# Kernel optimization log

Measured on AMD Instinct MI355X. Metric: run time of the kernel, lower is better.

The kernel has to match this reference:

```python
import jax, jax.numpy as jnp
import numpy as np

B, P, CIN, PS = 8192, 9, 12, 64   # batch, patches, channels, patch_size
D_IN = CIN * PS                    # 768 flattened patch features
ENC_H, D = 512, 1024               # patch_encoder_hidden, embedding_dim
E, EXP_H, C = 8, 2048, 1000        # num_experts, expert hidden, num_classes
SYM, SYM_H = 6, 64                 # symbolic_dim, symbolic gating hidden


def setup_inputs() -> dict:
    key = jax.random.key(0)
    ks = jax.random.split(key, 16)
    g = lambda k, shape, fan: jax.random.normal(k, shape, jnp.float32) / np.sqrt(fan)
    return {
        "patches": jax.random.normal(ks[0], (B, P, CIN, PS), jnp.float32),
        "symbolic_features": jax.random.normal(ks[1], (B, SYM), jnp.float32),
        # patch encoder (2-layer MLP per patch)
        "enc_w1": g(ks[2], (D_IN, ENC_H), D_IN), "enc_b1": jnp.zeros((ENC_H,), jnp.float32),
        "enc_w2": g(ks[3], (ENC_H, D), ENC_H),   "enc_b2": jnp.zeros((D,), jnp.float32),
        # neural gating: Linear(D,D)-ReLU-Linear(D,E)
        "gn_w1": g(ks[4], (D, D), D), "gn_b1": jnp.zeros((D,), jnp.float32),
        "gn_w2": g(ks[5], (D, E), D), "gn_b2": jnp.zeros((E,), jnp.float32),
        # symbolic gating: Linear(SYM,64)-ReLU-Linear(64,E)
        "gs_w1": g(ks[6], (SYM, SYM_H), SYM),  "gs_b1": jnp.zeros((SYM_H,), jnp.float32),
        "gs_w2": g(ks[7], (SYM_H, E), SYM_H),  "gs_b2": jnp.zeros((E,), jnp.float32),
        # stacked experts: Linear(D,H)-ReLU-(Dropout=eval identity)-Linear(H,C)
        "ew1": g(ks[8], (E, D, EXP_H), D),      "eb1": jnp.zeros((E, EXP_H), jnp.float32),
        "ew2": g(ks[9], (E, EXP_H, C), EXP_H),  "eb2": jnp.zeros((E, C), jnp.float32),
    }


def reference(patches, symbolic_features, enc_w1, enc_b1, enc_w2, enc_b2,
              gn_w1, gn_b1, gn_w2, gn_b2, gs_w1, gs_b1, gs_w2, gs_b2,
              ew1, eb1, ew2, eb2):
    b = patches.shape[0]
    # patch encoder: (b, P, CIN*PS) -> (b, P, D)
    x = patches.reshape(b, P, D_IN)
    h = jax.nn.relu(jnp.einsum('bpf,fh->bph', x, enc_w1) + enc_b1)
    encoded = jnp.einsum('bph,hd->bpd', h, enc_w2) + enc_b2
    # mean aggregation over patches
    agg = encoded.mean(axis=1)  # (b, D)
    # symbolic gating: 0.5*neural + 0.5*symbolic logits, softmax
    neural = jax.nn.relu(agg @ gn_w1 + gn_b1) @ gn_w2 + gn_b2            # (b, E)
    symb = jax.nn.relu(symbolic_features @ gs_w1 + gs_b1) @ gs_w2 + gs_b2  # (b, E)
    gating_weights = jax.nn.softmax(0.5 * neural + 0.5 * symb, axis=1)
    # all experts densely (batched over expert axis)
    eh = jax.nn.relu(jnp.einsum('bd,edh->beh', agg, ew1) + eb1)          # (b, E, H)
    expert_logits = jnp.einsum('beh,ehc->bec', eh, ew2) + eb2            # (b, E, C)
    # gate-weighted sum
    logits = jnp.einsum('be,bec->bc', gating_weights, expert_logits)     # (b, C)
    return logits, gating_weights, expert_logits
```

## Files before the change

### kernel.cpp

```cpp
#include <hip/hip_runtime.h>
#include <hip/hip_bf16.h>

typedef __attribute__((ext_vector_type(8))) short s16x8;
typedef __attribute__((ext_vector_type(4))) float f32x4;

#define DEV __device__ __forceinline__

DEV short f2b(float f) {
  __hip_bfloat16 h = __float2bfloat16(f);
  short s; __builtin_memcpy(&s, &h, 2); return s;
}
DEV float b2f(short s) {
  __hip_bfloat16 h; __builtin_memcpy(&h, &s, 2); return __bfloat162float(h);
}

typedef __attribute__((address_space(1))) const void gvoid;
typedef __attribute__((address_space(3))) void lvoid;
DEV void gload_lds16(const void* g, void* l) {
  __builtin_amdgcn_global_load_lds((gvoid*)g, (lvoid*)l, 16, 0, 0);
}

static constexpr int kB = 8192, kP = 9, kDIN = 768, kENCH = 512, kD = 1024;
static constexpr int kE = 8, kH = 2048, kC = 1000;
static constexpr size_t OUT_GATE   = (size_t)kB * kC;
static constexpr size_t OUT_EL     = OUT_GATE + (size_t)kB * kE;

static constexpr size_t W1T  = 0;
static constexpr size_t W2T  = W1T  + 786432;
static constexpr size_t GW1T = W2T  + 1048576;
static constexpr size_t EW1T = GW1T + 2097152;
static constexpr size_t EW2T = EW1T + 33554432;
static constexpr size_t PBF  = EW2T + 32768000;
static constexpr size_t HBUF = PBF  + 113246208;
static constexpr size_t EH4  = HBUF + 75497472;
static constexpr size_t HMEAN = PBF;
static constexpr size_t AGG   = HMEAN + 8388608;
static constexpr size_t GH    = AGG   + 16777216;
static constexpr size_t NEU   = GH    + 16777216;
static constexpr size_t SYMB  = NEU   + 262144;

__global__ void cast_bf16_kernel(const float* __restrict__ in, short* __restrict__ out, size_t n8) {
  size_t i = (size_t)blockIdx.x * blockDim.x + threadIdx.x;
  if (i >= n8) return;
  float4 a = ((const float4*)in)[i * 2];
  float4 b = ((const float4*)in)[i * 2 + 1];
  s16x8 v;
  v[0] = f2b(a.x); v[1] = f2b(a.y); v[2] = f2b(a.z); v[3] = f2b(a.w);
  v[4] = f2b(b.x); v[5] = f2b(b.y); v[6] = f2b(b.z); v[7] = f2b(b.w);
  *(s16x8*)(out + i * 8) = v;
}

__global__ void transpose_cast_kernel(const float* __restrict__ in, short* __restrict__ out,
                                      int R, int C, size_t istride, size_t ostride) {
  __shared__ float tile[32][33];
  const float* W = in + istride * blockIdx.z;
  short* T = out + ostride * blockIdx.z;
  int tx = threadIdx.x, ty = threadIdx.y;
  int c0 = blockIdx.x * 32, r0 = blockIdx.y * 32;
  #pragma unroll
  for (int i = 0; i < 32; i += 8) {
    int r = r0 + ty + i, c = c0 + tx;
    if (r < R && c < C) tile[ty + i][tx] = W[(size_t)r * C + c];
  }
  __syncthreads();
  #pragma unroll
  for (int i = 0; i < 32; i += 8) {
    int rr = c0 + ty + i, cc = r0 + tx;
    if (rr < C && cc < R) T[(size_t)rr * R + cc] = f2b(tile[tx][ty + i]);
  }
}

#define BARR() __builtin_amdgcn_s_barrier()
#define LGKM0() do { asm volatile("s_waitcnt lgkmcnt(0)" ::: "memory"); \
                     __builtin_amdgcn_sched_barrier(0); } while (0)
#define VMW4() asm volatile("s_waitcnt vmcnt(4)" ::: "memory")
#define VMW0() asm volatile("s_waitcnt vmcnt(0)" ::: "memory")

template<bool RELU, bool F32OUT, bool NTAIL>
__global__ __launch_bounds__(512, 2)
void gemm256_kernel(const short* __restrict__ A, const short* __restrict__ Bt,
                    const float* __restrict__ bias, void* __restrict__ Cout,
                    int M, int N, int K, int ldc,
                    long aZ, long bZ, long biasZ, long cZ) {
  __shared__ short Abuf[2][2][8192];
  __shared__ short Bbuf[2][2][8192];
  const int z = blockIdx.z;
  A += (size_t)z * aZ; Bt += (size_t)z * bZ; bias += (size_t)z * biasZ;

  const int XT = gridDim.x;
  int lid = blockIdx.y * XT + blockIdx.x;
  const int cpx = (XT * gridDim.y) >> 3;
  lid = (lid & 7) * cpx + (lid >> 3);
  const int bx = lid % XT, by = lid / XT;
  const int bM = by * 256, bN = bx * 256;

  const int t = threadIdx.x, lane = t & 63, wid = t >> 6;
  const int wm = wid & 1, wn = wid >> 1;
  const int lr = lane & 15, kg = lane >> 4;
  const int nkt = K >> 6;

  const int srB = t >> 3;
  const int sx = (t & 7) ^ (srB & 7);
  const int ldsoff = wid * 512;

#define STAGE_A(half, g_) do { \
    _Pragma("unroll") \
    for (int i_ = 0; i_ < 2; ++i_) { \
      int r_ = i_ * 64 + srB; \
      gload_lds16(A + (size_t)(bM + (half) * 128 + r_) * K + (g_) * 64 + sx * 8, \
                  &Abuf[(g_) & 1][half][i_ * 4096 + ldsoff]); \
    } } while (0)

#define STAGE_B(half, g_) do { \
    _Pragma("unroll") \
    for (int i_ = 0; i_ < 2; ++i_) { \
      int r_ = i_ * 64 + srB; \
      int row_ = bN + (half) * 128 + r_; \
      if (NTAIL && row_ >= N) row_ = N - 1; \
      gload_lds16(Bt + (size_t)row_ * K + (g_) * 64 + sx * 8, \
                  &Bbuf[(g_) & 1][half][i_ * 4096 + ldsoff]); \
    } } while (0)

  int aro = (wm * 64 + lr) * 64;
  int bro = (wn * 32 + lr) * 64;
  int so0 = ((0 * 4 + kg) ^ (lr & 7)) * 8;
  int so1 = ((1 * 4 + kg) ^ (lr & 7)) * 8;

  s16x8 af[4][2], bf[2][2];
#define LDA(mh, par_) do { \
    _Pragma("unroll") \
    for (int m_ = 0; m_ < 4; ++m_) { \
      af[m_][0] = *(const s16x8*)&Abuf[par_][mh][aro + m_ * 1024 + so0]; \
      af[m_][1] = *(const s16x8*)&Abuf[par_][mh][aro + m_ * 1024 + so1]; \
    } } while (0)
#define LDB(nh, par_) do { \
    _Pragma("unroll") \
    for (int n_ = 0; n_ < 2; ++n_) { \
      bf[n_][0] = *(const s16x8*)&Bbuf[par_][nh][bro + n_ * 1024 + so0]; \
      bf[n_][1] = *(const s16x8*)&Bbuf[par_][nh][bro + n_ * 1024 + so1]; \
    } } while (0)

  f32x4 acc[2][2][4][2];
  #pragma unroll
  for (int a_ = 0; a_ < 2; ++a_)
    #pragma unroll
    for (int b_ = 0; b_ < 2; ++b_)
      #pragma unroll
      for (int m_ = 0; m_ < 4; ++m_)
        #pragma unroll
        for (int n_ = 0; n_ < 2; ++n_) acc[a_][b_][m_][n_] = (f32x4){0.f, 0.f, 0.f, 0.f};

#define MMA(mh, nh) do { \
    __builtin_amdgcn_s_setprio(1); \
    _Pragma("unroll") \
    for (int m_ = 0; m_ < 4; ++m_) \
      _Pragma("unroll") \
      for (int n_ = 0; n_ < 2; ++n_) { \
        acc[mh][nh][m_][n_] = __builtin_amdgcn_mfma_f32_16x16x32_bf16(af[m_][0], bf[n_][0], acc[mh][nh][m_][n_], 0, 0, 0); \
        acc[mh][nh][m_][n_] = __builtin_amdgcn_mfma_f32_16x16x32_bf16(af[m_][1], bf[n_][1], acc[mh][nh][m_][n_], 0, 0, 0); \
      } \
    __builtin_amdgcn_s_setprio(0); } while (0)

  STAGE_A(0, 0); STAGE_B(0, 0); STAGE_B(1, 0); STAGE_A(1, 0);
  if (nkt > 1) { STAGE_A(0, 1); STAGE_B(1, 1); VMW4(); } else { VMW0(); }
  BARR();

  for (int g = 0; g < nkt; ++g) {
    const int par = g & 1;
    LDA(0, par); LDB(0, par);
    if (g + 1 < nkt) STAGE_B(0, g + 1);
    BARR(); LGKM0();
    MMA(0, 0);
    BARR();
    LDB(1, par);
    if (g + 1 < nkt) STAGE_A(1, g + 1);
    BARR(); LGKM0();
    MMA(0, 1);
    BARR();
    LDA(1, par);
    if (g + 2 < nkt) STAGE_A(0, g + 2);
    BARR(); LGKM0();
    MMA(1, 1);
    BARR();
    LDB(0, par);
    if (g + 2 < nkt) STAGE_B(1, g + 2);
    if (g < nkt - 2) { VMW4(); } else if (g == nkt - 2) { VMW0(); }
    BARR(); LGKM0();
    MMA(1, 0);
    BARR();
  }

  #pragma unroll
  for (int nh = 0; nh < 2; ++nh)
    #pragma unroll
    for (int n_ = 0; n_ < 2; ++n_) {
      int col = bN + nh * 128 + wn * 32 + n_ * 16 + lr;
      if (NTAIL && col >= N) continue;
      float bv = bias[col];
      #pragma unroll
      for (int mh = 0; mh < 2; ++mh)
        #pragma unroll
        for (int m_ = 0; m_ < 4; ++m_) {
          int row0 = bM + mh * 128 + wm * 64 + m_ * 16 + kg * 4;
          #pragma unroll
          for (int r_ = 0; r_ < 4; ++r_) {
            float v = acc[mh][nh][m_][n_][r_] + bv;
            if (RELU) v = fmaxf(v, 0.f);
            size_t off = (size_t)(row0 + r_) * ldc + col;
            if (F32OUT) ((float*)Cout + (size_t)z * cZ)[off] = v;
            else        ((short*)Cout + (size_t)z * cZ)[off] = f2b(v);
          }
        }
    }
#undef STAGE_A
#undef STAGE_B
#undef LDA
#undef LDB
#undef MMA
}

template<bool RELU, bool F32OUT>
__global__ __launch_bounds__(256, 2)
void gemm_bt_kernel(const short* __restrict__ A, const short* __restrict__ Bt,
                    const float* __restrict__ bias, void* __restrict__ Cout,
                    int M, int N, int K, int ldc) {
  __shared__ short As[128 * 32];
  __shared__ short Bs[128 * 32];
  const int t = threadIdx.x;
  const int lane = t & 63, wid = t >> 6;
  const int wr = wid >> 1, wc = wid & 1;
  const int lr = lane & 15, lk8 = (lane >> 4) * 8;
  const int arow0 = blockIdx.y * 128;
  const int bcol0 = blockIdx.x * 128;

  f32x4 acc[4][4];
  #pragma unroll
  for (int m = 0; m < 4; ++m)
    #pragma unroll
    for (int n = 0; n < 4; ++n) acc[m][n] = (f32x4){0.f, 0.f, 0.f, 0.f};

  const int srow = t >> 2, sseg = (t & 3) * 8;
  const short* ga0 = A + (size_t)(arow0 + srow) * K + sseg;
  const short* ga1 = ga0 + (size_t)64 * K;
  int br0 = bcol0 + srow;      if (br0 >= N) br0 = N - 1;
  int br1 = bcol0 + srow + 64; if (br1 >= N) br1 = N - 1;
  const short* gb0 = Bt + (size_t)br0 * K + sseg;
  const short* gb1 = Bt + (size_t)br1 * K + sseg;
  short* lA0 = As + wid * 512;
  short* lA1 = As + 2048 + wid * 512;
  short* lB0 = Bs + wid * 512;
  short* lB1 = Bs + 2048 + wid * 512;

  for (int k0 = 0; k0 < K; k0 += 32) {
    __syncthreads();
    gload_lds16(ga0, lA0);
    gload_lds16(ga1, lA1);
    gload_lds16(gb0, lB0);
    gload_lds16(gb1, lB1);
    ga0 += 32; ga1 += 32; gb0 += 32; gb1 += 32;
    __syncthreads();
    s16x8 af[4], bfr[4];
    #pragma unroll
    for (int m = 0; m < 4; ++m) af[m] = *(const s16x8*)&As[(wr * 64 + m * 16 + lr) * 32 + lk8];
    #pragma unroll
    for (int n = 0; n < 4; ++n) bfr[n] = *(const s16x8*)&Bs[(wc * 64 + n * 16 + lr) * 32 + lk8];
    #pragma unroll
    for (int m = 0; m < 4; ++m)
      #pragma unroll
      for (int n = 0; n < 4; ++n)
        acc[m][n] = __builtin_amdgcn_mfma_f32_16x16x32_bf16(af[m], bfr[n], acc[m][n], 0, 0, 0);
  }

  #pragma unroll
  for (int n = 0; n < 4; ++n) {
    int col = bcol0 + wc * 64 + n * 16 + lr;
    if (col >= N) continue;
    float bv = bias[col];
    #pragma unroll
    for (int m = 0; m < 4; ++m) {
      int row0 = arow0 + wr * 64 + m * 16 + (lane >> 4) * 4;
      #pragma unroll
      for (int r = 0; r < 4; ++r) {
        float v = acc[m][n][r] + bv;
        if (RELU) v = fmaxf(v, 0.f);
        size_t off = (size_t)(row0 + r) * ldc + col;
        if (F32OUT) ((float*)Cout)[off] = v;
        else        ((short*)Cout)[off] = f2b(v);
      }
    }
  }
}

__global__ void mean9_kernel(const short* __restrict__ h, short* __restrict__ hm) {
  size_t i = (size_t)blockIdx.x * blockDim.x + threadIdx.x;
  if (i >= (size_t)kB * kENCH / 8) return;
  size_t b = i >> 6; int d8 = (int)(i & 63);
  const short* base = h + b * kP * kENCH + d8 * 8;
  float s[8] = {0, 0, 0, 0, 0, 0, 0, 0};
  #pragma unroll
  for (int p = 0; p < kP; ++p) {
    s16x8 v = *(const s16x8*)(base + p * kENCH);
    #pragma unroll
    for (int j = 0; j < 8; ++j) s[j] += b2f(v[j]);
  }
  s16x8 o;
  #pragma unroll
  for (int j = 0; j < 8; ++j) o[j] = f2b(s[j] * (1.f / 9.f));
  *(s16x8*)(hm + i * 8) = o;
}

__global__ __launch_bounds__(256)
void gating_neural_kernel(const short* __restrict__ gh, const float* __restrict__ w2,
                          const float* __restrict__ b2, float* __restrict__ neural) {
  int wid = threadIdx.x >> 6, lane = threadIdx.x & 63;
  int row = blockIdx.x * 4 + wid;
  float acc[8] = {0,0,0,0,0,0,0,0};
  const short* grow = gh + (size_t)row * kD;
  for (int k = lane; k < kD; k += 64) {
    float x = b2f(grow[k]);
    const float* w = w2 + (size_t)k * 8;
    #pragma unroll
    for (int c = 0; c < 8; ++c) acc[c] += x * w[c];
  }
  #pragma unroll
  for (int c = 0; c < 8; ++c)
    #pragma unroll
    for (int off = 32; off >= 1; off >>= 1) acc[c] += __shfl_xor(acc[c], off);
  if (lane == 0) {
    #pragma unroll
    for (int c = 0; c < 8; ++c) neural[(size_t)row * 8 + c] = acc[c] + b2[c];
  }
}

__global__ __launch_bounds__(256)
void gating_symb_kernel(const float* __restrict__ sym, const float* __restrict__ w1,
                        const float* __restrict__ b1, const float* __restrict__ w2,
                        const float* __restrict__ b2, float* __restrict__ symb) {
  int wid = threadIdx.x >> 6, lane = threadIdx.x & 63;
  int row = blockIdx.x * 4 + wid;
  float s0 = sym[(size_t)row * 6 + 0], s1 = sym[(size_t)row * 6 + 1], s2 = sym[(size_t)row * 6 + 2];
  float s3 = sym[(size_t)row * 6 + 3], s4 = sym[(size_t)row * 6 + 4], s5 = sym[(size_t)row * 6 + 5];
  float hh = b1[lane];
  hh += s0 * w1[0 * 64 + lane] + s1 * w1[1 * 64 + lane] + s2 * w1[2 * 64 + lane];
  hh += s3 * w1[3 * 64 + lane] + s4 * w1[4 * 64 + lane] + s5 * w1[5 * 64 + lane];
  hh = fmaxf(hh, 0.f);
  float acc[8];
  #pragma unroll
  for (int c = 0; c < 8; ++c) acc[c] = hh * w2[lane * 8 + c];
  #pragma unroll
  for (int c = 0; c < 8; ++c)
    #pragma unroll
    for (int off = 32; off >= 1; off >>= 1) acc[c] += __shfl_xor(acc[c], off);
  if (lane == 0) {
    #pragma unroll
    for (int c = 0; c < 8; ++c) symb[(size_t)row * 8 + c] = acc[c] + b2[c];
  }
}

__global__ void gating_softmax_kernel(const float* __restrict__ neural, const float* __restrict__ symb,
                                      float* __restrict__ gate_out) {
  int row = blockIdx.x * blockDim.x + threadIdx.x;
  if (row >= kB) return;
  float g[8], m = -1e30f;
  #pragma unroll
  for (int c = 0; c < 8; ++c) {
    g[c] = 0.5f * (neural[(size_t)row * 8 + c] + symb[(size_t)row * 8 + c]);
    m = fmaxf(m, g[c]);
  }
  float sum = 0.f;
  #pragma unroll
  for (int c = 0; c < 8; ++c) { g[c] = expf(g[c] - m); sum += g[c]; }
  float inv = 1.f / sum;
  #pragma unroll
  for (int c = 0; c < 8; ++c) gate_out[(size_t)row * 8 + c] = g[c] * inv;
}

__global__ __launch_bounds__(256)
void combine_kernel(float* __restrict__ out) {
  int b = blockIdx.y;
  int c = blockIdx.x * 256 + threadIdx.x;
  __shared__ float g[8];
  if (threadIdx.x < 8) g[threadIdx.x] = out[OUT_GATE + (size_t)b * 8 + threadIdx.x];
  __syncthreads();
  if (c < kC) {
    const float* el = out + OUT_EL + (size_t)b * (kE * kC) + c;
    float a = 0.f;
    #pragma unroll
    for (int e = 0; e < 8; ++e) a += g[e] * el[e * kC];
    out[(size_t)b * kC + c] = a;
  }
}

static void launch_gemm128(bool relu, bool f32out, const short* A, const short* Bt, const float* bias,
                           void* C, int M, int N, int K, int ldc, hipStream_t s) {
  dim3 g((N + 127) / 128, M / 128), b(256);
  if (relu && !f32out)       gemm_bt_kernel<true,  false><<<g, b, 0, s>>>(A, Bt, bias, C, M, N, K, ldc);
  else if (!relu && !f32out) gemm_bt_kernel<false, false><<<g, b, 0, s>>>(A, Bt, bias, C, M, N, K, ldc);
  else if (relu && f32out)   gemm_bt_kernel<true,  true ><<<g, b, 0, s>>>(A, Bt, bias, C, M, N, K, ldc);
  else                       gemm_bt_kernel<false, true ><<<g, b, 0, s>>>(A, Bt, bias, C, M, N, K, ldc);
}

extern "C" void kernel_launch(void* const* d_in, const int* in_sizes, int n_in,
                              void* d_out, int out_size, void* d_ws, size_t ws_size,
                              hipStream_t stream) {
  const float* patches = (const float*)d_in[0];
  const float* symf    = (const float*)d_in[1];
  const float* enc_w1  = (const float*)d_in[2];
  const float* enc_b1  = (const float*)d_in[3];
  const float* enc_w2  = (const float*)d_in[4];
  const float* enc_b2  = (const float*)d_in[5];
  const float* gn_w1   = (const float*)d_in[6];
  const float* gn_b1   = (const float*)d_in[7];
  const float* gn_w2   = (const float*)d_in[8];
  const float* gn_b2   = (const float*)d_in[9];
  const float* gs_w1   = (const float*)d_in[10];
  const float* gs_b1   = (const float*)d_in[11];
  const float* gs_w2   = (const float*)d_in[12];
  const float* gs_b2   = (const float*)d_in[13];
  const float* ew1     = (const float*)d_in[14];
  const float* eb1     = (const float*)d_in[15];
  const float* ew2     = (const float*)d_in[16];
  const float* eb2     = (const float*)d_in[17];
  char* ws = (char*)d_ws;
  float* out = (float*)d_out;
  dim3 tb(32, 8);

  {
    size_t n8 = (size_t)kB * kP * kDIN / 8;
    cast_bf16_kernel<<<(unsigned)((n8 + 255) / 256), 256, 0, stream>>>(patches, (short*)(ws + PBF), n8);
  }
  transpose_cast_kernel<<<dim3(16, 24, 1), tb, 0, stream>>>(enc_w1, (short*)(ws + W1T),  kDIN,  kENCH, 0, 0);
  transpose_cast_kernel<<<dim3(32, 16, 1), tb, 0, stream>>>(enc_w2, (short*)(ws + W2T),  kENCH, kD,    0, 0);
  transpose_cast_kernel<<<dim3(32, 32, 1), tb, 0, stream>>>(gn_w1,  (short*)(ws + GW1T), kD,    kD,    0, 0);
  transpose_cast_kernel<<<dim3(64, 32, 8), tb, 0, stream>>>(ew1,    (short*)(ws + EW1T), kD,    kH,
                                                            (size_t)kD * kH, (size_t)kD * kH);
  transpose_cast_kernel<<<dim3(32, 64, 8), tb, 0, stream>>>(ew2,    (short*)(ws + EW2T), kH,    kC,
                                                            (size_t)kH * kC, (size_t)kH * kC);
  gemm256_kernel<true, false, false><<<dim3(2, 288, 1), 512, 0, stream>>>(
      (short*)(ws + PBF), (short*)(ws + W1T), enc_b1, ws + HBUF,
      kB * kP, kENCH, kDIN, kENCH, 0, 0, 0, 0);
  mean9_kernel<<<(kB * kENCH / 8) / 256, 256, 0, stream>>>((short*)(ws + HBUF), (short*)(ws + HMEAN));
  launch_gemm128(false, false, (short*)(ws + HMEAN), (short*)(ws + W2T), enc_b2,
                 ws + AGG, kB, kD, kENCH, kD, stream);
  launch_gemm128(true, false, (short*)(ws + AGG), (short*)(ws + GW1T), gn_b1,
                 ws + GH, kB, kD, kD, kD, stream);
  gating_neural_kernel<<<kB / 4, 256, 0, stream>>>((short*)(ws + GH), gn_w2, gn_b2, (float*)(ws + NEU));
  gating_symb_kernel<<<kB / 4, 256, 0, stream>>>(symf, gs_w1, gs_b1, gs_w2, gs_b2, (float*)(ws + SYMB));
  gating_softmax_kernel<<<kB / 256, 256, 0, stream>>>((float*)(ws + NEU), (float*)(ws + SYMB), out + OUT_GATE);
  for (int h = 0; h < 2; ++h) {
    int e0 = h * 4;
    gemm256_kernel<true, false, false><<<dim3(8, 32, 4), 512, 0, stream>>>(
        (short*)(ws + AGG), (short*)(ws + EW1T) + (size_t)e0 * kH * kD, eb1 + (size_t)e0 * kH,
        ws + EH4, kB, kH, kD, kH,
        0, (long)kH * kD, kH, (long)kB * kH);
    gemm256_kernel<false, true, true><<<dim3(4, 32, 4), 512, 0, stream>>>(
        (short*)(ws + EH4), (short*)(ws + EW2T) + (size_t)e0 * kC * kH, eb2 + (size_t)e0 * kC,
        out + OUT_EL + (size_t)e0 * kC, kB, kC, kH, kE * kC,
        (long)kB * kH, (long)kC * kH, kC, kC);
  }
  combine_kernel<<<dim3(4, kB), 256, 0, stream>>>(out);
}
```

Before: 1.033 ms.

## Keep B fragments in registers and issue unconditional prefetches with clamped indices

Gives the B fragment registers a per-half dimension so the final MMA(1,0) reuses the B(0) fragments loaded earlier, which drops one set of LDS reads per k-tile. Prefetch stages now always issue, with out-of-range tile indices clamped to the last tile. This keeps the number of outstanding loads constant so fixed vmcnt waits (8 and 6) can replace the conditional waits, placed at different points in the loop. It costs extra registers for the B fragments and some redundant global loads in the last iterations, and the new wait counts must exactly match the buffer reuse order to avoid races.

```diff
diff --git a/kernel.cpp b/kernel.cpp
--- a/kernel.cpp
+++ b/kernel.cpp
@@ -73,8 +73,8 @@
 #define BARR() __builtin_amdgcn_s_barrier()
 #define LGKM0() do { asm volatile("s_waitcnt lgkmcnt(0)" ::: "memory"); \
                      __builtin_amdgcn_sched_barrier(0); } while (0)
-#define VMW4() asm volatile("s_waitcnt vmcnt(4)" ::: "memory")
-#define VMW0() asm volatile("s_waitcnt vmcnt(0)" ::: "memory")
+#define VMW8() asm volatile("s_waitcnt vmcnt(8)" ::: "memory")
+#define VMW6() asm volatile("s_waitcnt vmcnt(6)" ::: "memory")
 
 template<bool RELU, bool F32OUT, bool NTAIL>
 __global__ __launch_bounds__(512, 2)
@@ -104,20 +104,22 @@
   const int ldsoff = wid * 512;
 
 #define STAGE_A(half, g_) do { \
+    int gc_ = (g_) < nkt ? (g_) : nkt - 1; \
     _Pragma("unroll") \
     for (int i_ = 0; i_ < 2; ++i_) { \
       int r_ = i_ * 64 + srB; \
-      gload_lds16(A + (size_t)(bM + (half) * 128 + r_) * K + (g_) * 64 + sx * 8, \
+      gload_lds16(A + (size_t)(bM + (half) * 128 + r_) * K + gc_ * 64 + sx * 8, \
                   &Abuf[(g_) & 1][half][i_ * 4096 + ldsoff]); \
     } } while (0)
 
 #define STAGE_B(half, g_) do { \
+    int gc_ = (g_) < nkt ? (g_) : nkt - 1; \
     _Pragma("unroll") \
     for (int i_ = 0; i_ < 2; ++i_) { \
       int r_ = i_ * 64 + srB; \
       int row_ = bN + (half) * 128 + r_; \
       if (NTAIL && row_ >= N) row_ = N - 1; \
-      gload_lds16(Bt + (size_t)row_ * K + (g_) * 64 + sx * 8, \
+      gload_lds16(Bt + (size_t)row_ * K + gc_ * 64 + sx * 8, \
                   &Bbuf[(g_) & 1][half][i_ * 4096 + ldsoff]); \
     } } while (0)
 
@@ -126,7 +128,7 @@
   int so0 = ((0 * 4 + kg) ^ (lr & 7)) * 8;
   int so1 = ((1 * 4 + kg) ^ (lr & 7)) * 8;
 
-  s16x8 af[4][2], bf[2][2];
+  s16x8 af[4][2], bf[2][2][2];
 #define LDA(mh, par_) do { \
     _Pragma("unroll") \
     for (int m_ = 0; m_ < 4; ++m_) { \
@@ -136,8 +138,8 @@
 #define LDB(nh, par_) do { \
     _Pragma("unroll") \
     for (int n_ = 0; n_ < 2; ++n_) { \
-      bf[n_][0] = *(const s16x8*)&Bbuf[par_][nh][bro + n_ * 1024 + so0]; \
-      bf[n_][1] = *(const s16x8*)&Bbuf[par_][nh][bro + n_ * 1024 + so1]; \
+      bf[nh][n_][0] = *(const s16x8*)&Bbuf[par_][nh][bro + n_ * 1024 + so0]; \
+      bf[nh][n_][1] = *(const s16x8*)&Bbuf[par_][nh][bro + n_ * 1024 + so1]; \
     } } while (0)
 
   f32x4 acc[2][2][4][2];
@@ -156,37 +158,38 @@
     for (int m_ = 0; m_ < 4; ++m_) \
       _Pragma("unroll") \
       for (int n_ = 0; n_ < 2; ++n_) { \
-        acc[mh][nh][m_][n_] = __builtin_amdgcn_mfma_f32_16x16x32_bf16(af[m_][0], bf[n_][0], acc[mh][nh][m_][n_], 0, 0, 0); \
-        acc[mh][nh][m_][n_] = __builtin_amdgcn_mfma_f32_16x16x32_bf16(af[m_][1], bf[n_][1], acc[mh][nh][m_][n_], 0, 0, 0); \
+        acc[mh][nh][m_][n_] = __builtin_amdgcn_mfma_f32_16x16x32_bf16(af[m_][0], bf[nh][n_][0], acc[mh][nh][m_][n_], 0, 0, 0); \
+        acc[mh][nh][m_][n_] = __builtin_amdgcn_mfma_f32_16x16x32_bf16(af[m_][1], bf[nh][n_][1], acc[mh][nh][m_][n_], 0, 0, 0); \
       } \
     __builtin_amdgcn_s_setprio(0); } while (0)
 
-  STAGE_A(0, 0); STAGE_B(0, 0); STAGE_B(1, 0); STAGE_A(1, 0);
-  if (nkt > 1) { STAGE_A(0, 1); STAGE_B(1, 1); VMW4(); } else { VMW0(); }
+  STAGE_A(0, 0); STAGE_B(1, 0); STAGE_B(0, 0); STAGE_A(1, 0);
+  STAGE_A(0, 1); STAGE_B(1, 1);
+  VMW6();
   BARR();
 
   for (int g = 0; g < nkt; ++g) {
     const int par = g & 1;
     LDA(0, par); LDB(0, par);
-    if (g + 1 < nkt) STAGE_B(0, g + 1);
+    STAGE_B(0, g + 1);
     BARR(); LGKM0();
     MMA(0, 0);
     BARR();
     LDB(1, par);
-    if (g + 1 < nkt) STAGE_A(1, g + 1);
+    STAGE_A(1, g + 1);
     BARR(); LGKM0();
     MMA(0, 1);
+    VMW8();
     BARR();
     LDA(1, par);
-    if (g + 2 < nkt) STAGE_A(0, g + 2);
+    STAGE_A(0, g + 2);
     BARR(); LGKM0();
     MMA(1, 1);
     BARR();
-    LDB(0, par);
-    if (g + 2 < nkt) STAGE_B(1, g + 2);
-    if (g < nkt - 2) { VMW4(); } else if (g == nkt - 2) { VMW0(); }
+    STAGE_B(1, g + 2);
     BARR(); LGKM0();
     MMA(1, 0);
+    VMW6();
     BARR();
   }
 
```

Result: slower. 1.122 ms (+8.6%).

## Keep separate A/B fragment registers and deepen global-to-LDS prefetch in 256 GEMM

Applied to the files above, without the earlier changes.

The 256x256 GEMM mainloop now holds separate register fragments for both A halves and both B halves, so the fourth quadrant reuses b0 instead of reloading it from LDS. Global-to-LDS staging is reordered so more tiles are issued ahead, with the vmcnt wait relaxed from 4 to 6 outstanding loads. Per-row global pointers are precomputed and incremented in place of recomputing addresses each stage. This aims to cut LDS reads and address arithmetic and to hide more memory latency, at the cost of extra VGPRs and pointer registers, which may pressure occupancy at launch bounds of 2 blocks of 512 threads.

```diff
diff --git a/kernel.cpp b/kernel.cpp
--- a/kernel.cpp
+++ b/kernel.cpp
@@ -73,6 +73,7 @@
 #define BARR() __builtin_amdgcn_s_barrier()
 #define LGKM0() do { asm volatile("s_waitcnt lgkmcnt(0)" ::: "memory"); \
                      __builtin_amdgcn_sched_barrier(0); } while (0)
+#define VMW6() asm volatile("s_waitcnt vmcnt(6)" ::: "memory")
 #define VMW4() asm volatile("s_waitcnt vmcnt(4)" ::: "memory")
 #define VMW0() asm volatile("s_waitcnt vmcnt(0)" ::: "memory")
 
@@ -103,41 +104,65 @@
   const int sx = (t & 7) ^ (srB & 7);
   const int ldsoff = wid * 512;
 
-#define STAGE_A(half, g_) do { \
-    _Pragma("unroll") \
-    for (int i_ = 0; i_ < 2; ++i_) { \
-      int r_ = i_ * 64 + srB; \
-      gload_lds16(A + (size_t)(bM + (half) * 128 + r_) * K + (g_) * 64 + sx * 8, \
-                  &Abuf[(g_) & 1][half][i_ * 4096 + ldsoff]); \
+  int ar0 = bM + srB, ar1 = bM + 64 + srB, ar2 = bM + 128 + srB, ar3 = bM + 192 + srB;
+  int br0 = bN + srB, br1 = bN + 64 + srB, br2 = bN + 128 + srB, br3 = bN + 192 + srB;
+  if (NTAIL) {
+    if (br0 >= N) br0 = N - 1;
+    if (br1 >= N) br1 = N - 1;
+    if (br2 >= N) br2 = N - 1;
+    if (br3 >= N) br3 = N - 1;
+  }
+  const short* pA00 = A + (size_t)ar0 * K + sx * 8;
+  const short* pA01 = A + (size_t)ar1 * K + sx * 8;
+  const short* pA10 = A + (size_t)ar2 * K + sx * 8;
+  const short* pA11 = A + (size_t)ar3 * K + sx * 8;
+  const short* pB00 = Bt + (size_t)br0 * K + sx * 8;
+  const short* pB01 = Bt + (size_t)br1 * K + sx * 8;
+  const short* pB10 = Bt + (size_t)br2 * K + sx * 8;
+  const short* pB11 = Bt + (size_t)br3 * K + sx * 8;
+
+#define STAGE_A0(tile_) do { if ((tile_) < nkt) { int par_ = (tile_) & 1; \
+    gload_lds16(pA00, &Abuf[par_][0][ldsoff]); \
+    gload_lds16(pA01, &Abuf[par_][0][4096 + ldsoff]); \
+    pA00 += 64; pA01 += 64; } } while (0)
+#define STAGE_A1(tile_) do { if ((tile_) < nkt) { int par_ = (tile_) & 1; \
+    gload_lds16(pA10, &Abuf[par_][1][ldsoff]); \
+    gload_lds16(pA11, &Abuf[par_][1][4096 + ldsoff]); \
+    pA10 += 64; pA11 += 64; } } while (0)
+#define STAGE_B0(tile_) do { if ((tile_) < nkt) { int par_ = (tile_) & 1; \
+    gload_lds16(pB00, &Bbuf[par_][0][ldsoff]); \
+    gload_lds16(pB01, &Bbuf[par_][0][4096 + ldsoff]); \
+    pB00 += 64; pB01 += 64; } } while (0)
+#define STAGE_B1(tile_) do { if ((tile_) < nkt) { int par_ = (tile_) & 1; \
+    gload_lds16(pB10, &Bbuf[par_][1][ldsoff]); \
+    gload_lds16(pB11, &Bbuf[par_][1][4096 + ldsoff]); \
+    pB10 += 64; pB11 += 64; } } while (0)
+
+  const int aro = (wm * 64 + lr) * 64;
+  const int bro = (wn * 32 + lr) * 64;
+  const int so0 = ((0 * 4 + kg) ^ (lr & 7)) * 8;
+  const int so1 = ((1 * 4 + kg) ^ (lr & 7)) * 8;
+
+  s16x8 a0[4][2], a1[4][2], b0[2][2], b1[2][2];
+#define LDA0(par_) do { _Pragma("unroll") \
+    for (int m_ = 0; m_ < 4; ++m_) { \
+      a0[m_][0] = *(const s16x8*)&Abuf[par_][0][aro + m_ * 1024 + so0]; \
+      a0[m_][1] = *(const s16x8*)&Abuf[par_][0][aro + m_ * 1024 + so1]; \
     } } while (0)
-
-#define STAGE_B(half, g_) do { \
-    _Pragma("unroll") \
-    for (int i_ = 0; i_ < 2; ++i_) { \
-      int r_ = i_ * 64 + srB; \
-      int row_ = bN + (half) * 128 + r_; \
-      if (NTAIL && row_ >= N) row_ = N - 1; \
-      gload_lds16(Bt + (size_t)row_ * K + (g_) * 64 + sx * 8, \
-                  &Bbuf[(g_) & 1][half][i_ * 4096 + ldsoff]); \
+#define LDA1(par_) do { _Pragma("unroll") \
+    for (int m_ = 0; m_ < 4; ++m_) { \
+      a1[m_][0] = *(const s16x8*)&Abuf[par_][1][aro + m_ * 1024 + so0]; \
+      a1[m_][1] = *(const s16x8*)&Abuf[par_][1][aro + m_ * 1024 + so1]; \
     } } while (0)
-
-  int aro = (wm * 64 + lr) * 64;
-  int bro = (wn * 32 + lr) * 64;
-  int so0 = ((0 * 4 + kg) ^ (lr & 7)) * 8;
-  int so1 = ((1 * 4 + kg) ^ (lr & 7)) * 8;
-
-  s16x8 af[4][2], bf[2][2];
-#define LDA(mh, par_) do { \
-    _Pragma("unroll") \
-    for (int m_ = 0; m_ < 4; ++m_) { \
-      af[m_][0] = *(const s16x8*)&Abuf[par_][mh][aro + m_ * 1024 + so0]; \
-      af[m_][1] = *(const s16x8*)&Abuf[par_][mh][aro + m_ * 1024 + so1]; \
+#define LDB0(par_) do { _Pragma("unroll") \
+    for (int n_ = 0; n_ < 2; ++n_) { \
+      b0[n_][0] = *(const s16x8*)&Bbuf[par_][0][bro + n_ * 1024 + so0]; \
+      b0[n_][1] = *(const s16x8*)&Bbuf[par_][0][bro + n_ * 1024 + so1]; \
     } } while (0)
-#define LDB(nh, par_) do { \
-    _Pragma("unroll") \
+#define LDB1(par_) do { _Pragma("unroll") \
     for (int n_ = 0; n_ < 2; ++n_) { \
-      bf[n_][0] = *(const s16x8*)&Bbuf[par_][nh][bro + n_ * 1024 + so0]; \
-      bf[n_][1] = *(const s16x8*)&Bbuf[par_][nh][bro + n_ * 1024 + so1]; \
+      b1[n_][0] = *(const s16x8*)&Bbuf[par_][1][bro + n_ * 1024 + so0]; \
+      b1[n_][1] = *(const s16x8*)&Bbuf[par_][1][bro + n_ * 1024 + so1]; \
     } } while (0)
 
   f32x4 acc[2][2][4][2];
@@ -150,43 +175,44 @@
         #pragma unroll
         for (int n_ = 0; n_ < 2; ++n_) acc[a_][b_][m_][n_] = (f32x4){0.f, 0.f, 0.f, 0.f};
 
-#define MMA(mh, nh) do { \
+#define MMAQ(mh, nh, AF, BF) do { \
     __builtin_amdgcn_s_setprio(1); \
     _Pragma("unroll") \
     for (int m_ = 0; m_ < 4; ++m_) \
       _Pragma("unroll") \
       for (int n_ = 0; n_ < 2; ++n_) { \
-        acc[mh][nh][m_][n_] = __builtin_amdgcn_mfma_f32_16x16x32_bf16(af[m_][0], bf[n_][0], acc[mh][nh][m_][n_], 0, 0, 0); \
-        acc[mh][nh][m_][n_] = __builtin_amdgcn_mfma_f32_16x16x32_bf16(af[m_][1], bf[n_][1], acc[mh][nh][m_][n_], 0, 0, 0); \
+        acc[mh][nh][m_][n_] = __builtin_amdgcn_mfma_f32_16x16x32_bf16(AF[m_][0], BF[n_][0], acc[mh][nh][m_][n_], 0, 0, 0); \
+        acc[mh][nh][m_][n_] = __builtin_amdgcn_mfma_f32_16x16x32_bf16(AF[m_][1], BF[n_][1], acc[mh][nh][m_][n_], 0, 0, 0); \
       } \
     __builtin_amdgcn_s_setprio(0); } while (0)
 
-  STAGE_A(0, 0); STAGE_B(0, 0); STAGE_B(1, 0); STAGE_A(1, 0);
-  if (nkt > 1) { STAGE_A(0, 1); STAGE_B(1, 1); VMW4(); } else { VMW0(); }
+  STAGE_A0(0); STAGE_B0(0); STAGE_B1(0); STAGE_A1(0);
+  VMW4();
+  STAGE_A0(1); STAGE_B0(1); STAGE_B1(1);
+  VMW6();
   BARR();
 
   for (int g = 0; g < nkt; ++g) {
     const int par = g & 1;
-    LDA(0, par); LDB(0, par);
-    if (g + 1 < nkt) STAGE_B(0, g + 1);
+    LDA0(par); LDB0(par);
+    STAGE_A1(g + 1);
     BARR(); LGKM0();
-    MMA(0, 0);
+    MMAQ(0, 0, a0, b0);
     BARR();
-    LDB(1, par);
-    if (g + 1 < nkt) STAGE_A(1, g + 1);
+    LDB1(par);
+    STAGE_A0(g + 2);
     BARR(); LGKM0();
-    MMA(0, 1);
+    MMAQ(0, 1, a0, b1);
     BARR();
-    LDA(1, par);
-    if (g + 2 < nkt) STAGE_A(0, g + 2);
+    LDA1(par);
+    STAGE_B0(g + 2);
     BARR(); LGKM0();
-    MMA(1, 1);
+    MMAQ(1, 1, a1, b1);
     BARR();
-    LDB(0, par);
-    if (g + 2 < nkt) STAGE_B(1, g + 2);
-    if (g < nkt - 2) { VMW4(); } else if (g == nkt - 2) { VMW0(); }
+    STAGE_B1(g + 2);
+    if (g == nkt - 2) { VMW0(); } else if (g < nkt - 2) { VMW6(); }
     BARR(); LGKM0();
-    MMA(1, 0);
+    MMAQ(1, 0, a1, b0);
     BARR();
   }
 
@@ -212,11 +238,15 @@
           }
         }
     }
-#undef STAGE_A
-#undef STAGE_B
-#undef LDA
-#undef LDB
-#undef MMA
+#undef STAGE_A0
+#undef STAGE_A1
+#undef STAGE_B0
+#undef STAGE_B1
+#undef LDA0
+#undef LDA1
+#undef LDB0
+#undef LDB1
+#undef MMAQ
 }
 
 template<bool RELU, bool F32OUT>
```

Result: no change. 1.016 ms (-1.7%).
